# Optimization experiments

Measured on AMD Instinct MI355X. Metric: run time of the kernel, lower is better.

Reference implementation:

```python
import math
import jax, jax.numpy as jnp
import numpy as np

E = 8          # num_experts
H = 1024       # hidden_dim
F = 2048       # ffn_dim
TOP_K = 2
CAP_FACTOR = 1.25
B, S = 2, 2048


def setup_inputs() -> dict:
    key = jax.random.key(0)
    ks = jax.random.split(key, 7)
    xavier_gu = math.sqrt(2.0 / (H + F))
    return {
        "x": jax.random.normal(ks[0], (B, S, H), dtype=jnp.float32),
        "router_weight": 0.01 * jax.random.normal(ks[1], (H, E), dtype=jnp.float32),
        "w_gate": xavier_gu * jax.random.normal(ks[2], (E, H, F), dtype=jnp.float32),
        "w_up": xavier_gu * jax.random.normal(ks[3], (E, H, F), dtype=jnp.float32),
        "w_down": xavier_gu * jax.random.normal(ks[4], (E, F, H), dtype=jnp.float32),
        "ln_gamma": jnp.ones((H,), dtype=jnp.float32),
        "ln_beta": jnp.zeros((H,), dtype=jnp.float32),
    }


def _layernorm(x, g, b, eps=1e-5):
    mu = x.mean(-1, keepdims=True)
    var = ((x - mu) ** 2).mean(-1, keepdims=True)
    return (x - mu) / jnp.sqrt(var + eps) * g + b


def reference(x, router_weight, w_gate, w_up, w_down, ln_gamma, ln_beta):
    Bd, Sd, Hd = x.shape
    T = Bd * Sd
    cap = int(math.ceil(CAP_FACTOR * T / E))  # static capacity per expert

    residual = x
    tokens = _layernorm(x, ln_gamma, ln_beta).reshape(T, Hd)

    # ---- router: softmax + top-k + renormalize ----
    logits = tokens @ router_weight                      # (T, E) fp32
    probs = jax.nn.softmax(logits, axis=-1)
    wts, idx = jax.lax.top_k(probs, TOP_K)               # (T, K)
    wts = wts / wts.sum(-1, keepdims=True)

    # ---- dispatch: first-come-first-served up to capacity per expert ----
    mask_all = (idx[None, :, :] == jnp.arange(E)[:, None, None]).any(-1)  # (E, T)
    # stable argsort puts routed token indices (in order) first
    sel = jnp.argsort(jnp.where(mask_all, 0, 1), axis=1, stable=True)[:, :cap]  # (E, cap)
    valid = jnp.take_along_axis(mask_all, sel, axis=1)   # (E, cap)
    xin = tokens[sel] * valid[..., None]                 # (E, cap, H); zeros for empty slots

    # ---- grouped SwiGLU expert GEMMs ----
    gate = jax.nn.silu(jnp.einsum('ech,ehf->ecf', xin, w_gate))
    up = jnp.einsum('ech,ehf->ecf', xin, w_up)
    expert_outputs = jnp.einsum('ecf,efh->ech', gate * up, w_down)  # (E, cap, H)

    # ---- scatter-gather combine (slot = min(t, cap-1), per reference impl) ----
    slot = jnp.minimum(jnp.arange(T), cap - 1)           # (T,)
    gathered = expert_outputs[idx, slot[:, None]]        # (T, K, H)
    out = (wts[..., None] * gathered).sum(axis=1)        # (T, H)

    return out.reshape(Bd, Sd, Hd) + residual
```

## Files before the change

### kernel.cpp

```cpp
#include <hip/hip_runtime.h>
#include <hip/hip_bf16.h>

#define NE 8
#define NH 1024
#define NF 2048
#define NT_TOK 4096
#define CAP 640

typedef __bf16 bf16x8 __attribute__((ext_vector_type(8)));
typedef float f32x4 __attribute__((ext_vector_type(4)));

__device__ __forceinline__ ushort f2bf(float f) {
    union { float f; unsigned u; } v; v.f = f;
    unsigned r = (v.u + 0x7FFFu + ((v.u >> 16) & 1u)) >> 16;
    return (ushort)r;
}

__device__ __forceinline__ void glds16(const ushort* g, ushort* l) {
    __builtin_amdgcn_global_load_lds((const __attribute__((address_space(1))) void*)g,
                                     (__attribute__((address_space(3))) void*)l,
                                     16, 0, 0);
}

#define MFMA_BF16 __builtin_amdgcn_mfma_f32_16x16x32_bf16

#define LR 132

__global__ __launch_bounds__(256) void k_conv_t(
    const float* __restrict__ wg, const float* __restrict__ wu,
    const float* __restrict__ wd, ushort* __restrict__ wgT,
    ushort* __restrict__ wuT, ushort* __restrict__ wdT)
{
    int z = blockIdx.z;
    const float* in; ushort* out; int R, C;
    if (z < 8)       { in = wg + (size_t)z * NH * NF;        out = wgT + (size_t)z * NH * NF;        R = NH; C = NF; }
    else if (z < 16) { in = wu + (size_t)(z - 8) * NH * NF;  out = wuT + (size_t)(z - 8) * NH * NF;  R = NH; C = NF; }
    else             { in = wd + (size_t)(z - 16) * NF * NH; out = wdT + (size_t)(z - 16) * NF * NH; R = NF; C = NH; }
    int c0 = blockIdx.x * 64, r0 = blockIdx.y * 128;
    if (c0 >= C || r0 >= R) return;

    __shared__ __align__(16) ushort lds[64 * LR];
    int tid = threadIdx.x;
    int rr = tid >> 4;
    int cc = (tid & 15) * 4;
    #pragma unroll
    for (int it = 0; it < 8; ++it) {
        int r = it * 16 + rr;
        float4 v = *(const float4*)(in + (size_t)(r0 + r) * C + c0 + cc);
        lds[(cc + 0) * LR + r] = f2bf(v.x);
        lds[(cc + 1) * LR + r] = f2bf(v.y);
        lds[(cc + 2) * LR + r] = f2bf(v.z);
        lds[(cc + 3) * LR + r] = f2bf(v.w);
    }
    __syncthreads();
    int cb = tid >> 5;
    int r4 = (tid & 31) * 4;
    #pragma unroll
    for (int it = 0; it < 8; ++it) {
        int cI = it * 8 + cb;
        uint2 v = *(const uint2*)&lds[cI * LR + r4];
        *(uint2*)(out + (size_t)(c0 + cI) * R + r0 + r4) = v;
    }
}

__global__ __launch_bounds__(256) void k_ln_router(
    const float* __restrict__ x, const float* __restrict__ rw,
    const float* __restrict__ gamma, const float* __restrict__ beta,
    ushort* __restrict__ tok_bf, int* __restrict__ idx, float* __restrict__ wts)
{
    int t = blockIdx.x, tid = threadIdx.x;
    int lane = tid & 63, wid = tid >> 6;
    const float* xp = x + (size_t)t * NH;

    float4 v = *(const float4*)(xp + tid * 4);
    float xs[4] = {v.x, v.y, v.z, v.w};
    float s = xs[0] + xs[1] + xs[2] + xs[3];
    float q = xs[0]*xs[0] + xs[1]*xs[1] + xs[2]*xs[2] + xs[3]*xs[3];

    __shared__ float rs[4], rq[4], rl[4][8];
    #pragma unroll
    for (int o = 32; o; o >>= 1) { s += __shfl_xor(s, o); q += __shfl_xor(q, o); }
    if (lane == 0) { rs[wid] = s; rq[wid] = q; }
    __syncthreads();
    float S = rs[0] + rs[1] + rs[2] + rs[3];
    float Q = rq[0] + rq[1] + rq[2] + rq[3];
    float mean = S * (1.0f / NH);
    float var  = Q * (1.0f / NH) - mean * mean;
    float rstd = 1.0f / sqrtf(var + 1e-5f);

    float le[8] = {0,0,0,0,0,0,0,0};
    ushort tb[4];
    #pragma unroll
    for (int j = 0; j < 4; ++j) {
        int h = tid * 4 + j;
        float nh = (xs[j] - mean) * rstd * gamma[h] + beta[h];
        tb[j] = f2bf(nh);
        float4 r0 = *(const float4*)(rw + h * 8);
        float4 r1 = *(const float4*)(rw + h * 8 + 4);
        le[0] += nh * r0.x; le[1] += nh * r0.y; le[2] += nh * r0.z; le[3] += nh * r0.w;
        le[4] += nh * r1.x; le[5] += nh * r1.y; le[6] += nh * r1.z; le[7] += nh * r1.w;
    }
    union { ushort s2[4]; uint2 u2; } pk;
    pk.s2[0]=tb[0]; pk.s2[1]=tb[1]; pk.s2[2]=tb[2]; pk.s2[3]=tb[3];
    *(uint2*)(tok_bf + (size_t)t * NH + tid * 4) = pk.u2;

    #pragma unroll
    for (int o = 32; o; o >>= 1)
        #pragma unroll
        for (int e = 0; e < 8; ++e) le[e] += __shfl_xor(le[e], o);
    if (lane == 0)
        #pragma unroll
        for (int e = 0; e < 8; ++e) rl[wid][e] = le[e];
    __syncthreads();

    if (tid == 0) {
        float l[8];
        #pragma unroll
        for (int e = 0; e < 8; ++e) l[e] = rl[0][e] + rl[1][e] + rl[2][e] + rl[3][e];
        float mx = l[0];
        #pragma unroll
        for (int e = 1; e < 8; ++e) mx = fmaxf(mx, l[e]);
        float p[8], den = 0.f;
        #pragma unroll
        for (int e = 0; e < 8; ++e) { p[e] = expf(l[e] - mx); den += p[e]; }
        float rden = 1.0f / den;
        #pragma unroll
        for (int e = 0; e < 8; ++e) p[e] *= rden;
        int i0 = 0; float b0 = p[0];
        #pragma unroll
        for (int e = 1; e < 8; ++e) if (p[e] > b0) { b0 = p[e]; i0 = e; }
        int i1 = (i0 == 0) ? 1 : 0; float b1 = p[i1];
        #pragma unroll
        for (int e = 0; e < 8; ++e) if (e != i0 && p[e] > b1) { b1 = p[e]; i1 = e; }
        float sw = 1.0f / (b0 + b1);
        idx[2*t] = i0; idx[2*t+1] = i1;
        wts[2*t] = b0 * sw; wts[2*t+1] = b1 * sw;
    }
}

__global__ __launch_bounds__(1024) void k_build_sel(
    const int* __restrict__ idx, int* __restrict__ sel)
{
    int e = blockIdx.x, tid = threadIdx.x;
    int lane = tid & 63, wid = tid >> 6;
    __shared__ int wsum[16], wpre[16], sbase;
    if (tid < CAP) sel[e * CAP + tid] = -1;
    if (tid == 0) sbase = 0;
    __syncthreads();

    for (int ch = 0; ch < NT_TOK / 1024; ++ch) {
        int t = ch * 1024 + tid;
        int m = (idx[2*t] == e || idx[2*t+1] == e) ? 1 : 0;
        int v = m;
        #pragma unroll
        for (int d = 1; d < 64; d <<= 1) {
            int u = __shfl_up(v, d);
            if (lane >= d) v += u;
        }
        if (lane == 63) wsum[wid] = v;
        __syncthreads();
        if (tid < 16) {
            int ws = wsum[tid], wv = ws;
            #pragma unroll
            for (int d = 1; d < 16; d <<= 1) {
                int u = __shfl_up(wv, d);
                if (tid >= d) wv += u;
            }
            wpre[tid] = wv - ws;
        }
        __syncthreads();
        int base0 = sbase;
        int slot = base0 + wpre[wid] + v - m;
        if (m && slot < CAP) sel[e * CAP + slot] = t;
        __syncthreads();
        if (tid == 0) sbase = base0 + wpre[15] + wsum[15];
        __syncthreads();
    }
}

__global__ __launch_bounds__(256) void k_gather(
    const int* __restrict__ sel, const ushort* __restrict__ tok,
    ushort* __restrict__ xin)
{
    int sIdx = blockIdx.x;
    int tokid = sel[sIdx];
    uint2 v = make_uint2(0u, 0u);
    if (tokid >= 0)
        v = *(const uint2*)(tok + (size_t)tokid * NH + threadIdx.x * 4);
    *(uint2*)(xin + (size_t)sIdx * NH + threadIdx.x * 4) = v;
}


__global__ __launch_bounds__(512, 4) void k_gemm1(
    const ushort* __restrict__ xin, const ushort* __restrict__ wgT,
    const ushort* __restrict__ wuT, ushort* __restrict__ hb)
{
    __shared__ __align__(16) ushort As[3][4096];
    __shared__ __align__(16) ushort Bgs[3][4096];
    __shared__ __align__(16) ushort Bus[3][4096];

    int e = blockIdx.z, mb = blockIdx.y, nb = blockIdx.x;
    const ushort* A  = xin + (size_t)e * CAP * NH + (size_t)mb * 128 * NH;
    const ushort* Bg = wgT + (size_t)e * NF * NH + (size_t)nb * 128 * NH;
    const ushort* Bu = wuT + (size_t)e * NF * NH + (size_t)nb * 128 * NH;

    int tid = threadIdx.x, lane = tid & 63, wid = tid >> 6;
    int wm = wid >> 2, wn = wid & 3;
    int lr = lane & 15, lq = lane >> 4;

    int Rg = tid >> 3;
    int ug = (tid & 7) ^ (Rg & 7);
    size_t goff = (size_t)(2 * Rg + (ug >> 2)) * NH + (ug & 3) * 8;
    int ldsu = tid * 8;

    int aoff[4], boff[2];
    #pragma unroll
    for (int m = 0; m < 4; ++m) {
        int a = wm * 64 + m * 16 + lr;
        int Rr = a >> 1;
        int sl = (((a & 1) << 2) | lq) ^ (Rr & 7);
        aoff[m] = Rr * 64 + sl * 8;
    }
    #pragma unroll
    for (int n = 0; n < 2; ++n) {
        int c = wn * 32 + n * 16 + lr;
        int Rr = c >> 1;
        int sl = (((c & 1) << 2) | lq) ^ (Rr & 7);
        boff[n] = Rr * 64 + sl * 8;
    }

    f32x4 accg[4][2] = {}; f32x4 accu[4][2] = {};
    const int NT = NH / 32;

    #define STG1(t, s) do { size_t _k = (size_t)(t) * 32;                       \
        glds16(A  + goff + _k, &As[s][ldsu]);                                   \
        glds16(Bg + goff + _k, &Bgs[s][ldsu]);                                  \
        glds16(Bu + goff + _k, &Bus[s][ldsu]); } while (0)

    STG1(0, 0); STG1(1, 1);
    asm volatile("s_waitcnt vmcnt(3)" ::: "memory");
    asm volatile("s_barrier" ::: "memory");

    int sl_c = 0, sl_p = 2;
    for (int t = 0; t < NT; ++t) {
        bool pf = (t + 2 < NT);
        if (pf) STG1(t + 2, sl_p);
        const ushort* Ab = &As[sl_c][0];
        const ushort* Gb = &Bgs[sl_c][0];
        const ushort* Ub = &Bus[sl_c][0];
        bf16x8 af[4], bg[2], bu[2];
        #pragma unroll
        for (int m = 0; m < 4; ++m) af[m] = *(const bf16x8*)&Ab[aoff[m]];
        #pragma unroll
        for (int n = 0; n < 2; ++n) {
            bg[n] = *(const bf16x8*)&Gb[boff[n]];
            bu[n] = *(const bf16x8*)&Ub[boff[n]];
        }
        __builtin_amdgcn_s_setprio(1);
        #pragma unroll
        for (int m = 0; m < 4; ++m)
            #pragma unroll
            for (int n = 0; n < 2; ++n) {
                accg[m][n] = MFMA_BF16(af[m], bg[n], accg[m][n], 0, 0, 0);
                accu[m][n] = MFMA_BF16(af[m], bu[n], accu[m][n], 0, 0, 0);
            }
        __builtin_amdgcn_s_setprio(0);
        if (pf) asm volatile("s_waitcnt vmcnt(3)" ::: "memory");
        else    asm volatile("s_waitcnt vmcnt(0)" ::: "memory");
        asm volatile("s_barrier" ::: "memory");
        sl_c = (sl_c == 2) ? 0 : sl_c + 1;
        sl_p = (sl_p == 2) ? 0 : sl_p + 1;
    }
    #undef STG1

    ushort* outp = hb + (size_t)e * CAP * NF + (size_t)mb * 128 * NF + nb * 128;
    #pragma unroll
    for (int m = 0; m < 4; ++m)
        #pragma unroll
        for (int n = 0; n < 2; ++n)
            #pragma unroll
            for (int r = 0; r < 4; ++r) {
                int row = wm * 64 + m * 16 + lq * 4 + r;
                int col = wn * 32 + n * 16 + lr;
                float g = accg[m][n][r], u = accu[m][n][r];
                float sg = g / (1.0f + expf(-g));
                outp[(size_t)row * NF + col] = f2bf(sg * u);
            }
}

__global__ __launch_bounds__(256, 4) void k_gemm2(
    const ushort* __restrict__ hb, const ushort* __restrict__ wdT,
    float* __restrict__ eo)
{
    __shared__ __align__(16) ushort As[3][4096];
    __shared__ __align__(16) ushort Bs[3][4096];

    int e = blockIdx.z, mb = blockIdx.y, nb = blockIdx.x;
    const ushort* A = hb  + (size_t)e * CAP * NF + (size_t)mb * 128 * NF;
    const ushort* B = wdT + (size_t)e * NH * NF + (size_t)nb * 128 * NF;

    int tid = threadIdx.x, lane = tid & 63, wid = tid >> 6;
    int wm = wid >> 1, wn = wid & 1;
    int lr = lane & 15, lq = lane >> 4;

    int Rg = tid >> 3;
    int ug = (tid & 7) ^ (Rg & 7);
    int sROW2 = ug >> 2, sCOL = (ug & 3) * 8;
    size_t goff0 = (size_t)(2 * Rg + sROW2) * NF + sCOL;
    size_t goff1 = (size_t)(2 * (32 + Rg) + sROW2) * NF + sCOL;
    int ldsu = tid * 8;

    int aoff[4], boff[4];
    #pragma unroll
    for (int m = 0; m < 4; ++m) {
        int a = wm * 64 + m * 16 + lr;
        int Rr = a >> 1;
        int sl = (((a & 1) << 2) | lq) ^ (Rr & 7);
        aoff[m] = Rr * 64 + sl * 8;
    }
    #pragma unroll
    for (int n = 0; n < 4; ++n) {
        int c = wn * 64 + n * 16 + lr;
        int Rr = c >> 1;
        int sl = (((c & 1) << 2) | lq) ^ (Rr & 7);
        boff[n] = Rr * 64 + sl * 8;
    }

    f32x4 acc[4][4] = {};
    const int NT = NF / 32;

    #define STG2(t, s) do { size_t _k = (size_t)(t) * 32;                       \
        glds16(A + goff0 + _k, &As[s][ldsu]);                                   \
        glds16(A + goff1 + _k, &As[s][2048 + ldsu]);                            \
        glds16(B + goff0 + _k, &Bs[s][ldsu]);                                   \
        glds16(B + goff1 + _k, &Bs[s][2048 + ldsu]); } while (0)

    STG2(0, 0); STG2(1, 1);
    asm volatile("s_waitcnt vmcnt(4)" ::: "memory");
    asm volatile("s_barrier" ::: "memory");

    int sl_c = 0, sl_p = 2;
    for (int t = 0; t < NT; ++t) {
        bool pf = (t + 2 < NT);
        if (pf) STG2(t + 2, sl_p);
        const ushort* Ab = &As[sl_c][0];
        const ushort* Bb = &Bs[sl_c][0];
        bf16x8 af[4], bf_[4];
        #pragma unroll
        for (int m = 0; m < 4; ++m) af[m] = *(const bf16x8*)&Ab[aoff[m]];
        #pragma unroll
        for (int n = 0; n < 4; ++n) bf_[n] = *(const bf16x8*)&Bb[boff[n]];
        __builtin_amdgcn_s_setprio(1);
        #pragma unroll
        for (int m = 0; m < 4; ++m)
            #pragma unroll
            for (int n = 0; n < 4; ++n)
                acc[m][n] = MFMA_BF16(af[m], bf_[n], acc[m][n], 0, 0, 0);
        __builtin_amdgcn_s_setprio(0);
        if (pf) asm volatile("s_waitcnt vmcnt(4)" ::: "memory");
        else    asm volatile("s_waitcnt vmcnt(0)" ::: "memory");
        asm volatile("s_barrier" ::: "memory");
        sl_c = (sl_c == 2) ? 0 : sl_c + 1;
        sl_p = (sl_p == 2) ? 0 : sl_p + 1;
    }
    #undef STG2

    float* outp = eo + (size_t)e * CAP * NH + (size_t)mb * 128 * NH + nb * 128;
    #pragma unroll
    for (int m = 0; m < 4; ++m)
        #pragma unroll
        for (int n = 0; n < 4; ++n)
            #pragma unroll
            for (int r = 0; r < 4; ++r) {
                int row = wm * 64 + m * 16 + lq * 4 + r;
                int col = wn * 64 + n * 16 + lr;
                outp[(size_t)row * NH + col] = acc[m][n][r];
            }
}

__global__ __launch_bounds__(256) void k_final(
    const float* __restrict__ x, const float* __restrict__ eo,
    const int* __restrict__ idx, const float* __restrict__ wts,
    float* __restrict__ out)
{
    int t = blockIdx.x;
    int c = (t < CAP - 1) ? t : (CAP - 1);
    int e0 = idx[2*t], e1 = idx[2*t+1];
    float w0 = wts[2*t], w1 = wts[2*t+1];
    int h = threadIdx.x * 4;
    float4 xv = *(const float4*)(x + (size_t)t * NH + h);
    float4 a = *(const float4*)(eo + ((size_t)e0 * CAP + c) * NH + h);
    float4 b = *(const float4*)(eo + ((size_t)e1 * CAP + c) * NH + h);
    float4 o;
    o.x = xv.x + w0 * a.x + w1 * b.x;
    o.y = xv.y + w0 * a.y + w1 * b.y;
    o.z = xv.z + w0 * a.z + w1 * b.z;
    o.w = xv.w + w0 * a.w + w1 * b.w;
    *(float4*)(out + (size_t)t * NH + h) = o;
}

extern "C" void kernel_launch(void* const* d_in, const int* in_sizes, int n_in,
                              void* d_out, int out_size, void* d_ws, size_t ws_size,
                              hipStream_t stream)
{
    const float* x     = (const float*)d_in[0];
    const float* rw    = (const float*)d_in[1];
    const float* wg    = (const float*)d_in[2];
    const float* wu    = (const float*)d_in[3];
    const float* wd    = (const float*)d_in[4];
    const float* gamma = (const float*)d_in[5];
    const float* beta  = (const float*)d_in[6];
    float* out = (float*)d_out;

    char* ws = (char*)d_ws;
    float*  eo     = (float*) (ws);
    ushort* tok_bf = (ushort*)(ws);
    ushort* xin    = (ushort*)(ws +  20971520);
    ushort* hb     = (ushort*)(ws +  31457280);
    ushort* wgT    = (ushort*)(ws +  52428800);
    ushort* wuT    = (ushort*)(ws +  85983232);
    ushort* wdT    = (ushort*)(ws + 119537664);
    int*    idx    = (int*)   (ws + 153092096);
    float*  wts    = (float*) (ws + 153124864);
    int*    sel    = (int*)   (ws + 153157632);

    k_conv_t<<<dim3(32, 16, 24), 256, 0, stream>>>(wg, wu, wd, wgT, wuT, wdT);

    k_ln_router<<<NT_TOK, 256, 0, stream>>>(x, rw, gamma, beta, tok_bf, idx, wts);
    k_build_sel<<<NE, 1024, 0, stream>>>(idx, sel);
    k_gather<<<NE * CAP, 256, 0, stream>>>(sel, tok_bf, xin);
    k_gemm1<<<dim3(NF / 128, CAP / 128, NE), 512, 0, stream>>>(xin, wgT, wuT, hb);
    k_gemm2<<<dim3(NH / 128, CAP / 128, NE), 256, 0, stream>>>(hb, wdT, eo);
    k_final<<<NT_TOK, 256, 0, stream>>>(x, eo, idx, wts, out);
}
```

Before: 383.5 us.

## Enlarge gemm1 tile, pad capacity, swizzle block order, rework weight transpose

The gate/up GEMM moves to 256-row tiles, with gate and up weight rows interleaved into a single B tile and a four-stage LDS ring whose loads are split into quarter-step phases between barriers. Capacity is padded to 768 rows so the tiles divide evenly. Both GEMMs use a flattened grid with a block-index swizzle so that co-scheduled blocks share expert weights. The weight conversion/transpose kernel now uses an XOR-swizzled LDS layout with 16-byte stores and is split into two launches. The larger tile raises reuse but lowers occupancy, and the padding adds wasted rows to the gather and to gemm1.

Result: slower. 423.9 us (+10.5%).

```diff
diff --git a/kernel.cpp b/kernel.cpp
--- a/kernel.cpp
+++ b/kernel.cpp
@@ -6,6 +6,7 @@
 #define NF 2048
 #define NT_TOK 4096
 #define CAP 640
+#define CAPP 768
 
 typedef __bf16 bf16x8 __attribute__((ext_vector_type(8)));
 typedef float f32x4 __attribute__((ext_vector_type(4)));
@@ -24,42 +25,46 @@
 
 #define MFMA_BF16 __builtin_amdgcn_mfma_f32_16x16x32_bf16
 
-#define LR 132
-
 __global__ __launch_bounds__(256) void k_conv_t(
-    const float* __restrict__ wg, const float* __restrict__ wu,
-    const float* __restrict__ wd, ushort* __restrict__ wgT,
-    ushort* __restrict__ wuT, ushort* __restrict__ wdT)
+    const float* __restrict__ inA, const float* __restrict__ inB,
+    ushort* __restrict__ outA, ushort* __restrict__ outB, int R, int C)
 {
     int z = blockIdx.z;
-    const float* in; ushort* out; int R, C;
-    if (z < 8)       { in = wg + (size_t)z * NH * NF;        out = wgT + (size_t)z * NH * NF;        R = NH; C = NF; }
-    else if (z < 16) { in = wu + (size_t)(z - 8) * NH * NF;  out = wuT + (size_t)(z - 8) * NH * NF;  R = NH; C = NF; }
-    else             { in = wd + (size_t)(z - 16) * NF * NH; out = wdT + (size_t)(z - 16) * NF * NH; R = NF; C = NH; }
+    const float* in = (z & 8) ? inB : inA;
+    ushort* out = (z & 8) ? outB : outA;
+    int e = z & 7;
+    in  += (size_t)e * R * C;
+    out += (size_t)e * R * C;
     int c0 = blockIdx.x * 64, r0 = blockIdx.y * 128;
-    if (c0 >= C || r0 >= R) return;
-
-    __shared__ __align__(16) ushort lds[64 * LR];
-    int tid = threadIdx.x;
-    int rr = tid >> 4;
-    int cc = (tid & 15) * 4;
+
+    __shared__ __align__(16) ushort lds[128 * 64];
+    int t = threadIdx.x;
+    int rr = t >> 4;
+    int ci = t & 15;
     #pragma unroll
     for (int it = 0; it < 8; ++it) {
         int r = it * 16 + rr;
-        float4 v = *(const float4*)(in + (size_t)(r0 + r) * C + c0 + cc);
-        lds[(cc + 0) * LR + r] = f2bf(v.x);
-        lds[(cc + 1) * LR + r] = f2bf(v.y);
-        lds[(cc + 2) * LR + r] = f2bf(v.z);
-        lds[(cc + 3) * LR + r] = f2bf(v.w);
+        float4 v = *(const float4*)(in + (size_t)(r0 + r) * C + c0 + ci * 4);
+        union { ushort sh[4]; uint2 u; } p;
+        p.sh[0] = f2bf(v.x); p.sh[1] = f2bf(v.y);
+        p.sh[2] = f2bf(v.z); p.sh[3] = f2bf(v.w);
+        int slot = ci ^ ((r >> 3) & 15);
+        *(uint2*)&lds[r * 64 + slot * 4] = p.u;
     }
     __syncthreads();
-    int cb = tid >> 5;
-    int r4 = (tid & 31) * 4;
-    #pragma unroll
-    for (int it = 0; it < 8; ++it) {
-        int cI = it * 8 + cb;
-        uint2 v = *(const uint2*)&lds[cI * LR + r4];
-        *(uint2*)(out + (size_t)(c0 + cI) * R + r0 + r4) = v;
+    int g  = t >> 4;
+    int ra = t & 15;
+    #pragma unroll
+    for (int it = 0; it < 4; ++it) {
+        int c = it * 16 + g;
+        int ca = c >> 2, cw = c & 3;
+        union { ushort sh[8]; uint4 u; } p;
+        #pragma unroll
+        for (int j = 0; j < 8; ++j) {
+            int r = ra * 8 + j;
+            p.sh[j] = lds[r * 64 + ((ca ^ ((r >> 3) & 15)) << 2) + cw];
+        }
+        *(uint4*)(out + (size_t)(c0 + c) * R + r0 + ra * 8) = p.u;
     }
 }
 
@@ -144,7 +149,7 @@
     int e = blockIdx.x, tid = threadIdx.x;
     int lane = tid & 63, wid = tid >> 6;
     __shared__ int wsum[16], wpre[16], sbase;
-    if (tid < CAP) sel[e * CAP + tid] = -1;
+    if (tid < CAPP) sel[e * CAPP + tid] = -1;
     if (tid == 0) sbase = 0;
     __syncthreads();
 
@@ -171,7 +176,7 @@
         __syncthreads();
         int base0 = sbase;
         int slot = base0 + wpre[wid] + v - m;
-        if (m && slot < CAP) sel[e * CAP + slot] = t;
+        if (m && slot < CAP) sel[e * CAPP + slot] = t;
         __syncthreads();
         if (tid == 0) sbase = base0 + wpre[15] + wsum[15];
         __syncthreads();
@@ -190,99 +195,136 @@
     *(uint2*)(xin + (size_t)sIdx * NH + threadIdx.x * 4) = v;
 }
 
-
-__global__ __launch_bounds__(512, 4) void k_gemm1(
+__global__ __launch_bounds__(512, 2) void k_gemm1(
     const ushort* __restrict__ xin, const ushort* __restrict__ wgT,
     const ushort* __restrict__ wuT, ushort* __restrict__ hb)
 {
-    __shared__ __align__(16) ushort As[3][4096];
-    __shared__ __align__(16) ushort Bgs[3][4096];
-    __shared__ __align__(16) ushort Bus[3][4096];
-
-    int e = blockIdx.z, mb = blockIdx.y, nb = blockIdx.x;
-    const ushort* A  = xin + (size_t)e * CAP * NH + (size_t)mb * 128 * NH;
-    const ushort* Bg = wgT + (size_t)e * NF * NH + (size_t)nb * 128 * NH;
-    const ushort* Bu = wuT + (size_t)e * NF * NH + (size_t)nb * 128 * NH;
-
-    int tid = threadIdx.x, lane = tid & 63, wid = tid >> 6;
+    __shared__ __align__(16) ushort As[4][8192];
+    __shared__ __align__(16) ushort Bs[4][8192];
+
+    int bid = blockIdx.x;
+    int sw = (bid & 7) * 48 + (bid >> 3);
+    int e  = sw / 48;
+    int r48 = sw % 48;
+    int mb = r48 >> 4, nb = r48 & 15;
+
+    const ushort* A  = xin + (size_t)e * CAPP * NH + (size_t)mb * 256 * NH;
+    int f0 = nb * 128;
+    const ushort* Wg = wgT + (size_t)e * NF * NH;
+    const ushort* Wu = wuT + (size_t)e * NF * NH;
+
+    int tid = threadIdx.x, lane = tid & 63;
+    int wid = tid >> 6;
     int wm = wid >> 2, wn = wid & 3;
     int lr = lane & 15, lq = lane >> 4;
 
-    int Rg = tid >> 3;
-    int ug = (tid & 7) ^ (Rg & 7);
-    size_t goff = (size_t)(2 * Rg + (ug >> 2)) * NH + (ug & 3) * 8;
-    int ldsu = tid * 8;
-
-    int aoff[4], boff[2];
-    #pragma unroll
-    for (int m = 0; m < 4; ++m) {
-        int a = wm * 64 + m * 16 + lr;
-        int Rr = a >> 1;
-        int sl = (((a & 1) << 2) | lq) ^ (Rr & 7);
-        aoff[m] = Rr * 64 + sl * 8;
-    }
-    #pragma unroll
-    for (int n = 0; n < 2; ++n) {
-        int c = wn * 32 + n * 16 + lr;
-        int Rr = c >> 1;
-        int sl = (((c & 1) << 2) | lq) ^ (Rr & 7);
-        boff[n] = Rr * 64 + sl * 8;
-    }
-
-    f32x4 accg[4][2] = {}; f32x4 accu[4][2] = {};
+    int ar = tid >> 2;
+    int tch = (tid & 3) ^ ((tid >> 3) & 3);
+    int scol = tch * 8;
+    const ushort* srcA0 = A + (size_t)ar * NH + scol;
+    const ushort* srcA1 = A + (size_t)(128 + ar) * NH + scol;
+    int b0 = ar, b1 = 128 + ar;
+    const ushort* srcB0 = (((b0 >> 5) & 1) ? Wu : Wg)
+        + (size_t)(f0 + ((b0 >> 6) << 5) + (b0 & 31)) * NH + scol;
+    const ushort* srcB1 = (((b1 >> 5) & 1) ? Wu : Wg)
+        + (size_t)(f0 + ((b1 >> 6) << 5) + (b1 & 31)) * NH + scol;
+    int dl = tid * 8;
+
+    int aoff[8], boff[4];
+    #pragma unroll
+    for (int m = 0; m < 8; ++m) {
+        int a = wm * 128 + m * 16 + lr;
+        aoff[m] = (a * 4 + (lq ^ ((a >> 1) & 3))) * 8;
+    }
+    #pragma unroll
+    for (int n = 0; n < 4; ++n) {
+        int b = wn * 64 + n * 16 + lr;
+        boff[n] = (b * 4 + (lq ^ ((b >> 1) & 3))) * 8;
+    }
+
+    f32x4 acc[8][4] = {};
     const int NT = NH / 32;
 
-    #define STG1(t, s) do { size_t _k = (size_t)(t) * 32;                       \
-        glds16(A  + goff + _k, &As[s][ldsu]);                                   \
-        glds16(Bg + goff + _k, &Bgs[s][ldsu]);                                  \
-        glds16(Bu + goff + _k, &Bus[s][ldsu]); } while (0)
-
-    STG1(0, 0); STG1(1, 1);
-    asm volatile("s_waitcnt vmcnt(3)" ::: "memory");
-    asm volatile("s_barrier" ::: "memory");
-
-    int sl_c = 0, sl_p = 2;
+    glds16(srcA0,      &As[0][dl]);
+    glds16(srcA1,      &As[0][4096 + dl]);
+    glds16(srcB0,      &Bs[0][dl]);
+    glds16(srcB1,      &Bs[0][4096 + dl]);
+    glds16(srcA0 + 32, &As[1][dl]);
+    glds16(srcA1 + 32, &As[1][4096 + dl]);
+    glds16(srcB0 + 32, &Bs[1][dl]);
+    glds16(srcB1 + 32, &Bs[1][4096 + dl]);
+    asm volatile("s_waitcnt vmcnt(4)" ::: "memory");
+    __builtin_amdgcn_s_barrier();
+
     for (int t = 0; t < NT; ++t) {
+        int buf = t & 3, sb = (t + 2) & 3;
         bool pf = (t + 2 < NT);
-        if (pf) STG1(t + 2, sl_p);
-        const ushort* Ab = &As[sl_c][0];
-        const ushort* Gb = &Bgs[sl_c][0];
-        const ushort* Ub = &Bus[sl_c][0];
-        bf16x8 af[4], bg[2], bu[2];
-        #pragma unroll
-        for (int m = 0; m < 4; ++m) af[m] = *(const bf16x8*)&Ab[aoff[m]];
-        #pragma unroll
-        for (int n = 0; n < 2; ++n) {
-            bg[n] = *(const bf16x8*)&Gb[boff[n]];
-            bu[n] = *(const bf16x8*)&Ub[boff[n]];
-        }
+        size_t ko = (size_t)(t + 2) * 32;
+        const ushort* Ab = &As[buf][0];
+        const ushort* Bb = &Bs[buf][0];
+        bf16x8 af0[4], af1[4], bf0[2], bf1[2];
+
+        if (pf) glds16(srcA0 + ko, &As[sb][dl]);
+        #pragma unroll
+        for (int m = 0; m < 4; ++m) af0[m] = *(const bf16x8*)&Ab[aoff[m]];
+        #pragma unroll
+        for (int n = 0; n < 2; ++n) bf0[n] = *(const bf16x8*)&Bb[boff[n]];
         __builtin_amdgcn_s_setprio(1);
         #pragma unroll
         for (int m = 0; m < 4; ++m)
             #pragma unroll
-            for (int n = 0; n < 2; ++n) {
-                accg[m][n] = MFMA_BF16(af[m], bg[n], accg[m][n], 0, 0, 0);
-                accu[m][n] = MFMA_BF16(af[m], bu[n], accu[m][n], 0, 0, 0);
-            }
+            for (int n = 0; n < 2; ++n)
+                acc[m][n] = MFMA_BF16(af0[m], bf0[n], acc[m][n], 0, 0, 0);
         __builtin_amdgcn_s_setprio(0);
-        if (pf) asm volatile("s_waitcnt vmcnt(3)" ::: "memory");
+        __builtin_amdgcn_s_barrier();
+
+        if (pf) glds16(srcA1 + ko, &As[sb][4096 + dl]);
+        #pragma unroll
+        for (int m = 0; m < 4; ++m) af1[m] = *(const bf16x8*)&Ab[aoff[4 + m]];
+        __builtin_amdgcn_s_setprio(1);
+        #pragma unroll
+        for (int m = 0; m < 4; ++m)
+            #pragma unroll
+            for (int n = 0; n < 2; ++n)
+                acc[4 + m][n] = MFMA_BF16(af1[m], bf0[n], acc[4 + m][n], 0, 0, 0);
+        __builtin_amdgcn_s_setprio(0);
+        __builtin_amdgcn_s_barrier();
+
+        if (pf) glds16(srcB0 + ko, &Bs[sb][dl]);
+        #pragma unroll
+        for (int n = 0; n < 2; ++n) bf1[n] = *(const bf16x8*)&Bb[boff[2 + n]];
+        __builtin_amdgcn_s_setprio(1);
+        #pragma unroll
+        for (int m = 0; m < 4; ++m)
+            #pragma unroll
+            for (int n = 0; n < 2; ++n)
+                acc[4 + m][2 + n] = MFMA_BF16(af1[m], bf1[n], acc[4 + m][2 + n], 0, 0, 0);
+        __builtin_amdgcn_s_setprio(0);
+        __builtin_amdgcn_s_barrier();
+
+        if (pf) glds16(srcB1 + ko, &Bs[sb][4096 + dl]);
+        __builtin_amdgcn_s_setprio(1);
+        #pragma unroll
+        for (int m = 0; m < 4; ++m)
+            #pragma unroll
+            for (int n = 0; n < 2; ++n)
+                acc[m][2 + n] = MFMA_BF16(af0[m], bf1[n], acc[m][2 + n], 0, 0, 0);
+        __builtin_amdgcn_s_setprio(0);
+        if (pf) asm volatile("s_waitcnt vmcnt(4)" ::: "memory");
         else    asm volatile("s_waitcnt vmcnt(0)" ::: "memory");
-        asm volatile("s_barrier" ::: "memory");
-        sl_c = (sl_c == 2) ? 0 : sl_c + 1;
-        sl_p = (sl_p == 2) ? 0 : sl_p + 1;
-    }
-    #undef STG1
-
-    ushort* outp = hb + (size_t)e * CAP * NF + (size_t)mb * 128 * NF + nb * 128;
-    #pragma unroll
-    for (int m = 0; m < 4; ++m)
+        __builtin_amdgcn_s_barrier();
+    }
+
+    ushort* outp = hb + (size_t)e * CAPP * NF + (size_t)(mb * 256) * NF + f0;
+    #pragma unroll
+    for (int m = 0; m < 8; ++m)
         #pragma unroll
         for (int n = 0; n < 2; ++n)
             #pragma unroll
             for (int r = 0; r < 4; ++r) {
-                int row = wm * 64 + m * 16 + lq * 4 + r;
+                int row = wm * 128 + m * 16 + lq * 4 + r;
                 int col = wn * 32 + n * 16 + lr;
-                float g = accg[m][n][r], u = accu[m][n][r];
+                float g = acc[m][n][r], u = acc[m][n + 2][r];
                 float sg = g / (1.0f + expf(-g));
                 outp[(size_t)row * NF + col] = f2bf(sg * u);
             }
@@ -295,8 +337,13 @@
     __shared__ __align__(16) ushort As[3][4096];
     __shared__ __align__(16) ushort Bs[3][4096];
 
-    int e = blockIdx.z, mb = blockIdx.y, nb = blockIdx.x;
-    const ushort* A = hb  + (size_t)e * CAP * NF + (size_t)mb * 128 * NF;
+    int bid = blockIdx.x;
+    int sw = (bid & 7) * 40 + (bid >> 3);
+    int e = sw / 40;
+    int r40 = sw % 40;
+    int mb = r40 >> 3, nb = r40 & 7;
+
+    const ushort* A = hb  + (size_t)e * CAPP * NF + (size_t)mb * 128 * NF;
     const ushort* B = wdT + (size_t)e * NH * NF + (size_t)nb * 128 * NF;
 
     int tid = threadIdx.x, lane = tid & 63, wid = tid >> 6;
@@ -416,20 +463,21 @@
     float*  eo     = (float*) (ws);
     ushort* tok_bf = (ushort*)(ws);
     ushort* xin    = (ushort*)(ws +  20971520);
-    ushort* hb     = (ushort*)(ws +  31457280);
-    ushort* wgT    = (ushort*)(ws +  52428800);
-    ushort* wuT    = (ushort*)(ws +  85983232);
-    ushort* wdT    = (ushort*)(ws + 119537664);
-    int*    idx    = (int*)   (ws + 153092096);
-    float*  wts    = (float*) (ws + 153124864);
-    int*    sel    = (int*)   (ws + 153157632);
-
-    k_conv_t<<<dim3(32, 16, 24), 256, 0, stream>>>(wg, wu, wd, wgT, wuT, wdT);
+    ushort* hb     = (ushort*)(ws +  33554432);
+    ushort* wgT    = (ushort*)(ws +  58720256);
+    ushort* wuT    = (ushort*)(ws +  92274688);
+    ushort* wdT    = (ushort*)(ws + 125829120);
+    int*    idx    = (int*)   (ws + 159383552);
+    float*  wts    = (float*) (ws + 159416320);
+    int*    sel    = (int*)   (ws + 159449088);
+
+    k_conv_t<<<dim3(NF / 64, NH / 128, 16), 256, 0, stream>>>(wg, wu, wgT, wuT, NH, NF);
+    k_conv_t<<<dim3(NH / 64, NF / 128, 8),  256, 0, stream>>>(wd, wd, wdT, wdT, NF, NH);
 
     k_ln_router<<<NT_TOK, 256, 0, stream>>>(x, rw, gamma, beta, tok_bf, idx, wts);
     k_build_sel<<<NE, 1024, 0, stream>>>(idx, sel);
-    k_gather<<<NE * CAP, 256, 0, stream>>>(sel, tok_bf, xin);
-    k_gemm1<<<dim3(NF / 128, CAP / 128, NE), 512, 0, stream>>>(xin, wgT, wuT, hb);
-    k_gemm2<<<dim3(NH / 128, CAP / 128, NE), 256, 0, stream>>>(hb, wdT, eo);
+    k_gather<<<NE * CAPP, 256, 0, stream>>>(sel, tok_bf, xin);
+    k_gemm1<<<384, 512, 0, stream>>>(xin, wgT, wuT, hb);
+    k_gemm2<<<320, 256, 0, stream>>>(hb, wdT, eo);
     k_final<<<NT_TOK, 256, 0, stream>>>(x, eo, idx, wts, out);
 }
```
